# Optimization experiments

Hardware: AMD Instinct MI355X
Metric: run time of the kernel (lower is better)

Reference implementation:

```python
import jax, jax.numpy as jnp
import numpy as np

N, E, D, H, C = 50000, 250000, 300, 4, 75  # nodes, edges, in_size=300, heads=4, out=75 (H*C=300)


def setup_inputs() -> dict:
    key = jax.random.key(0)
    ks = jax.random.split(key, 32)
    rn = lambda k, shape, s=0.05: jax.random.normal(k, shape, jnp.float32) * s
    inp = {}
    inp['x'] = rn(ks[0], (N, D), 1.0)
    inp['edge_index'] = jax.random.randint(ks[1], (2, E), 0, N, dtype=jnp.int32)
    inp['edge_attr'] = rn(ks[2], (E, 4), 1.0)
    inp['obj_normals'] = rn(ks[3], (N, 3), 1.0)
    # parameters (Linear stored as [in, out] so y = x @ W + b)
    inp['Wq'] = rn(ks[4], (D, H * C)); inp['bq'] = rn(ks[5], (H * C,))
    inp['Wk'] = rn(ks[6], (D, H * C)); inp['bk'] = rn(ks[7], (H * C,))
    inp['Wv'] = rn(ks[8], (D, H * C)); inp['bv'] = rn(ks[9], (H * C,))
    inp['We'] = rn(ks[10], (D, H * C))               # lin_edge, no bias
    inp['Wn'] = rn(ks[11], (3, D)); inp['bn'] = rn(ks[12], (D,))      # map_normal
    inp['Wxy'] = rn(ks[13], (2, D)); inp['bxy'] = rn(ks[14], (D,))    # map_xy_relative_coord
    inp['Wloc'] = rn(ks[15], (3 * D, D)); inp['bloc'] = rn(ks[16], (D,))  # map_back_edge_loc
    inp['Wobj'] = rn(ks[17], (2 * D, D)); inp['bobj'] = rn(ks[18], (D,))  # map_back_edge_obj
    inp['Wfus'] = rn(ks[19], (2 * D, D)); inp['bfus'] = rn(ks[20], (D,))  # hv_words_fusion
    inp['Wcls'] = rn(ks[21], (D, 5)); inp['bcls'] = rn(ks[22], (5,))      # horizontal_word_cls
    inp['Wskip'] = rn(ks[23], (D, H * C)); inp['bskip'] = rn(ks[24], (H * C,))  # lin_skip
    inp['vocab'] = rn(ks[25], (7, D), 1.0)  # spatial_vocab_we
    return inp


def reference(x, edge_index, edge_attr, obj_normals,
              Wq, bq, Wk, bk, Wv, bv, We, Wn, bn, Wxy, bxy,
              Wloc, bloc, Wobj, bobj, Wfus, bfus, Wcls, bcls,
              Wskip, bskip, vocab):
    src, dst = edge_index[0], edge_index[1]  # x_j = x[src], x_i = x[dst]
    x_i = x[dst]
    x_j = x[src]
    q = (x_i @ Wq + bq).reshape(E, H, C)
    k = (x_j @ Wk + bk).reshape(E, H, C)
    # vertical (top/bottom) word embeddings gated by edge_attr signs
    top = (edge_attr[:, 0] > 0).astype(x.dtype)[:, None] * vocab[0][None, :]
    bot = (edge_attr[:, 1] < 0).astype(x.dtype)[:, None] * vocab[1][None, :]
    vert = top + bot                                           # [E, D]
    # horizontal word probabilities from geometry + feature cues
    ni = obj_normals[dst] @ Wn + bn
    nj = obj_normals[src] @ Wn + bn
    xy = edge_attr[:, 2:4] @ Wxy + bxy
    loc = jnp.concatenate([xy, ni, nj], axis=1) @ Wloc + bloc
    obj = jnp.concatenate([x_i, x_j - x_i], axis=1) @ Wobj + bobj
    prob = jax.nn.softmax(jnp.tanh(obj + loc) @ Wcls + bcls, axis=1)   # [E, 5]
    horiz = prob @ vocab[2:7]                                  # [E, D]
    edge_word = jnp.concatenate([vert, horiz], axis=1) @ Wfus + bfus   # [E, D]
    ef = (edge_word @ We).reshape(E, H, C)                     # lin_edge
    k = k + ef
    # scaled dot-product attention with per-destination-node softmax
    alpha = (q * k).sum(-1) / jnp.asarray(np.sqrt(C), x.dtype)  # [E, H]
    m = jax.ops.segment_max(alpha, dst, num_segments=N)
    alpha = jnp.exp(alpha - m[dst])
    den = jax.ops.segment_sum(alpha, dst, num_segments=N)
    alpha = alpha / den[dst]
    v = (x_j @ Wv + bv).reshape(E, H, C) + ef
    msg = v * alpha[..., None]                                  # [E, H, C]
    out = jax.ops.segment_sum(msg, dst, num_segments=N).reshape(N, H * C)
    out = out + x @ Wskip + bskip                               # concat heads + root skip
    return out
```

## Files before the change

### kernel.cpp

```cpp
#include <hip/hip_runtime.h>
#include <hip/hip_bf16.h>
#include <math.h>

#define NDIM 300
#define KPAD 320
#define NREAL 1800
#define NPAD 1920

typedef __hip_bfloat16 bf16;
typedef __attribute__((ext_vector_type(8))) short short8;
typedef __attribute__((ext_vector_type(4))) float f32x4;

__device__ __forceinline__ void gl_lds16(const void* g, void* l) {
    __builtin_amdgcn_global_load_lds(
        (const __attribute__((address_space(1))) void*)g,
        (__attribute__((address_space(3))) void*)l, 16, 0, 0);
}

__device__ __forceinline__ float bflo(uint u) { return __uint_as_float(u << 16); }
__device__ __forceinline__ float bfhi(uint u) { return __uint_as_float(u & 0xFFFF0000u); }

__global__ void small_pre(
    const float* __restrict__ Wn, const float* __restrict__ bn,
    const float* __restrict__ Wxy, const float* __restrict__ bxy,
    const float* __restrict__ Wloc, const float* __restrict__ bloc,
    const float* __restrict__ bobj,
    const float* __restrict__ Wfus,
    const float* __restrict__ vocab,
    float* __restrict__ Wn1, float* __restrict__ Wn2,
    float* __restrict__ Mxy, float* __restrict__ bgeo,
    float* __restrict__ vf5, float* __restrict__ t0, float* __restrict__ t1)
{
    int i = blockIdx.x * blockDim.x + threadIdx.x;
    if (i < 900) {
        int r = i / 300, c = i % 300;
        float s = 0.f;
        for (int k = 0; k < 300; k++) s += Wn[r*300+k] * Wloc[(300+k)*300+c];
        Wn1[i] = s;
    } else if (i < 1800) {
        int j = i - 900; int r = j/300, c = j%300;
        float s = 0.f;
        for (int k = 0; k < 300; k++) s += Wn[r*300+k] * Wloc[(600+k)*300+c];
        Wn2[j] = s;
    } else if (i < 2400) {
        int j = i - 1800; int r = j/300, c = j%300;
        float s = 0.f;
        for (int k = 0; k < 300; k++) s += Wxy[r*300+k] * Wloc[k*300+c];
        Mxy[j] = 2.f * s;
    } else if (i < 2700) {
        int c = i - 2400;
        float s = bloc[c] + bobj[c];
        for (int k = 0; k < 300; k++) s += bxy[k] * Wloc[k*300+c];
        for (int k = 0; k < 300; k++) s += bn[k] * (Wloc[(300+k)*300+c] + Wloc[(600+k)*300+c]);
        bgeo[c] = 2.f * s;
    } else if (i < 4200) {
        int j = i - 2700; int p = j/300, c = j%300;
        float s = 0.f;
        for (int k = 0; k < 300; k++) s += vocab[(2+p)*300+k] * Wfus[(300+k)*300+c];
        vf5[j] = s;
    } else if (i < 4500) {
        int c = i - 4200;
        float s = 0.f;
        for (int k = 0; k < 300; k++) s += vocab[k] * Wfus[k*300+c];
        t0[c] = s;
    } else if (i < 4800) {
        int c = i - 4500;
        float s = 0.f;
        for (int k = 0; k < 300; k++) s += vocab[300+k] * Wfus[k*300+c];
        t1[c] = s;
    }
}

__global__ void small_pre2(
    const float* __restrict__ We, const float* __restrict__ bfus,
    const float* __restrict__ vf5, const float* __restrict__ t0, const float* __restrict__ t1,
    const float* __restrict__ Wcls,
    float* __restrict__ E8, float* __restrict__ WclsT)
{
    int i = blockIdx.x * blockDim.x + threadIdx.x;
    if (i < 2400) {
        int r = i / 300, c = i % 300;
        const float* src;
        if (r == 0) src = t0;
        else if (r == 1) src = t1;
        else if (r == 7) src = bfus;
        else src = vf5 + (r - 2) * 300;
        float s = 0.f;
        for (int k = 0; k < 300; k++) s += src[k] * We[k*300+c];
        E8[i] = s;
    } else if (i < 3900) {
        int j = i - 2400; int cl = j / 300, c = j % 300;
        WclsT[cl * 300 + c] = Wcls[c * 5 + cl];
    }
}

__global__ void pack_w(
    const float* __restrict__ Wq, const float* __restrict__ Wk,
    const float* __restrict__ Wv, const float* __restrict__ Wskip,
    const float* __restrict__ Wobj,
    const float* __restrict__ Wn1, const float* __restrict__ Wn2,
    const float* __restrict__ bq, const float* __restrict__ bk,
    const float* __restrict__ bv, const float* __restrict__ bskip,
    bf16* __restrict__ WcatT, float* __restrict__ bcat)
{
    int i = blockIdx.x * blockDim.x + threadIdx.x;
    if (i < NREAL) {
        int c = i;
        float b = 0.f;
        if (c < 600)       { if (!(c & 1)) b = bq[c >> 1]; }
        else if (c < 1200) { int cc = c - 600; if (cc & 1) b = bk[cc >> 1]; }
        else if (c < 1500) b = bv[c - 1200];
        else               b = bskip[c - 1500];
        bcat[i] = b;
    }
    if (i < NPAD * KPAD) {
        int cp = i / KPAD, k = i % KPAD;
        float v = 0.f;
        if (cp < NREAL) {
            int seg, jj;
            if (cp < 600)       { jj = cp >> 1; seg = (cp & 1) ? 4 : 0; }
            else if (cp < 1200) { int cc = cp - 600; jj = cc >> 1; seg = (cc & 1) ? 1 : 5; }
            else if (cp < 1500) { jj = cp - 1200; seg = 2; }
            else                { jj = cp - 1500; seg = 3; }
            if (k < 300) {
                switch (seg) {
                    case 0: v = Wq[k*300+jj]; break;
                    case 1: v = Wk[k*300+jj]; break;
                    case 2: v = Wv[k*300+jj]; break;
                    case 3: v = Wskip[k*300+jj]; break;
                    case 4: v = Wobj[k*300+jj] - Wobj[(300+k)*300+jj]; break;
                    default: v = Wobj[(300+k)*300+jj]; break;
                }
            } else if (k < 303) {
                if (seg == 4) v = Wn1[(k-300)*300+jj];
                else if (seg == 5) v = Wn2[(k-300)*300+jj];
            }
            if (seg >= 4) v *= 2.f;
        }
        WcatT[i] = __float2bfloat16(v);
    }
}

__global__ void conv_xb(const float* __restrict__ X, const float* __restrict__ Nrm,
                        bf16* __restrict__ Xb, int M)
{
    int i = blockIdx.x * blockDim.x + threadIdx.x;
    int row = i / 40, c8 = i % 40;
    if (row >= M) return;
    int c0 = c8 * 8;
    union { bf16 h[8]; short8 s; } u;
    #pragma unroll
    for (int t = 0; t < 8; t++) {
        int c = c0 + t;
        float v = 0.f;
        if (c < 300)      v = X[(size_t)row * 300 + c];
        else if (c < 303) v = Nrm[(size_t)row * 3 + (c - 300)];
        u.h[t] = __float2bfloat16(v);
    }
    *(short8*)&Xb[(size_t)row * 320 + c0] = u.s;
}

__global__ __launch_bounds__(256) void qe8_k(
    const bf16* __restrict__ QP, const float* __restrict__ E8,
    float* __restrict__ QE8f, int N)
{
    __shared__ unsigned short Qs[64 * 302];
    const int tid = threadIdx.x;
    const int n0 = blockIdx.x * 64;
    const int nrows = min(64, N - n0);
    const int nu = nrows * 300;
    const uint* src = (const uint*)QP + (size_t)n0 * 300;
    for (int i = tid; i < nu; i += 256) {
        int rr = i / 300, cc = i - rr * 300;
        Qs[rr * 302 + cc] = (unsigned short)src[i];
    }
    __syncthreads();
    const int w = tid >> 6, l = tid & 63;
    if (l >= nrows) return;
    float acc[8] = {0.f,0.f,0.f,0.f,0.f,0.f,0.f,0.f};
    const int cb = 75 * w;
    for (int cc = 0; cc < 75; cc++) {
        int c = cb + cc;
        float qv = __uint_as_float(((uint)Qs[l * 302 + c]) << 16);
        #pragma unroll
        for (int s = 0; s < 8; s++) acc[s] += qv * E8[s * 300 + c];
    }
    float* out = QE8f + (size_t)(n0 + l) * 32;
    #pragma unroll
    for (int s = 0; s < 8; s++) out[s * 4 + w] = acc[s];
}

__global__ void hist_k(const int* __restrict__ ei, int* __restrict__ deg, int E) {
    int e = blockIdx.x * blockDim.x + threadIdx.x;
    if (e < E) atomicAdd(&deg[ei[E + e]], 1);
}

__global__ __launch_bounds__(1024) void scan_local(
    const int* __restrict__ deg, int* __restrict__ off, int* __restrict__ bsum, int N)
{
    __shared__ int buf[1024];
    int i = blockIdx.x * 1024 + threadIdx.x;
    int v = (i < N) ? deg[i] : 0;
    buf[threadIdx.x] = v;
    __syncthreads();
    #pragma unroll
    for (int ofs = 1; ofs < 1024; ofs <<= 1) {
        int t = (threadIdx.x >= ofs) ? buf[threadIdx.x - ofs] : 0;
        __syncthreads();
        buf[threadIdx.x] += t;
        __syncthreads();
    }
    if (i < N) off[i] = buf[threadIdx.x] - v;
    if (threadIdx.x == 1023) bsum[blockIdx.x] = buf[1023];
}

__global__ __launch_bounds__(1024) void scan_bsum(
    const int* __restrict__ bsum, int* __restrict__ bexc, int nb)
{
    __shared__ int buf[1024];
    int v = (threadIdx.x < nb) ? bsum[threadIdx.x] : 0;
    buf[threadIdx.x] = v;
    __syncthreads();
    #pragma unroll
    for (int ofs = 1; ofs < 1024; ofs <<= 1) {
        int t = (threadIdx.x >= ofs) ? buf[threadIdx.x - ofs] : 0;
        __syncthreads();
        buf[threadIdx.x] += t;
        __syncthreads();
    }
    if (threadIdx.x < nb) bexc[threadIdx.x] = buf[threadIdx.x] - v;
}

__global__ void scan_add(int* __restrict__ off, int* __restrict__ cur,
                         const int* __restrict__ bexc, int N, int E)
{
    int i = blockIdx.x * blockDim.x + threadIdx.x;
    if (i < N) {
        int o = off[i] + bexc[i >> 10];
        off[i] = o; cur[i] = o;
    }
    if (i == 0) off[N] = E;
}

__global__ void scatter_k(const int* __restrict__ ei, const float* __restrict__ ea,
                          int* __restrict__ cur,
                          int2* __restrict__ esd, float* __restrict__ eas, int E) {
    int e = blockIdx.x * blockDim.x + threadIdx.x;
    if (e < E) {
        int s = ei[e];
        int d = ei[E + e];
        float4 a = *(const float4*)&ea[(size_t)e * 4];
        int p = atomicAdd(&cur[d], 1);
        esd[p] = make_int2(s, d);
        *(float4*)&eas[(size_t)p * 4] = a;
    }
}

__global__ __launch_bounds__(256) void gemm_mfma(
    const bf16* __restrict__ Xb,
    const bf16* __restrict__ Bt, const float* __restrict__ bcat,
    bf16* __restrict__ QP, bf16* __restrict__ PK, bf16* __restrict__ V,
    float* __restrict__ Ot, int M, int npan)
{
    __shared__ __align__(16) char smraw[32768];
    bf16*  Asb = (bf16*)smraw;
    bf16*  Bsb = (bf16*)(smraw + 16384);
    bf16*  EP  = (bf16*)smraw;
    float* EPf = (float*)smraw;

    const int bid = blockIdx.x;
    int p, cx;
    {
        const int full = (npan >> 3) * 120;
        if (bid < full) {
            int g = bid / 120, r = bid - g * 120;
            p = (g << 3) + (r & 7); cx = r >> 3;
        } else {
            int r = bid - full;
            int tp = npan & 7;
            p = (npan & ~7) + r % tp; cx = r / tp;
        }
    }
    const int r0 = p * 128;
    const int c0 = cx * 128;

    const int tid  = threadIdx.x;
    const int wave = tid >> 6;
    const int lane = tid & 63;
    const int wm = (wave >> 1) * 64;
    const int wn = (wave & 1) * 64;
    const int lr = lane & 15;
    const int lq = lane >> 4;

    f32x4 acc[4][4];
    #pragma unroll
    for (int j = 0; j < 4; j++)
        #pragma unroll
        for (int i = 0; i < 4; i++) acc[j][i] = (f32x4){0.f, 0.f, 0.f, 0.f};

    const bf16* aSrc[2];
    const bf16* bSrc[2];
    {
        const int bcol_l = lane >> 2;
        const int bkp    = (lane & 3) * 8;
        #pragma unroll
        for (int h = 0; h < 2; h++) {
            int t = h * 256 + wave * 64 + lane;
            int grow = min(r0 + (t >> 2), M - 1);
            aSrc[h] = Xb + (size_t)grow * 320 + (t & 3) * 8;
            bSrc[h] = Bt + (size_t)(c0 + wave * 32 + h * 16 + bcol_l) * KPAD + bkp;
        }
    }

    auto stage = [&](int buf, int kb) {
        #pragma unroll
        for (int h = 0; h < 2; h++) {
            int tbase = h * 256 + wave * 64;
            gl_lds16(aSrc[h] + kb, &Asb[buf * 4096 + tbase * 8]);
        }
        #pragma unroll
        for (int h = 0; h < 2; h++) {
            int cloc = wave * 32 + h * 16;
            gl_lds16(bSrc[h] + kb, &Bsb[buf * 4096 + cloc * 32]);
        }
    };

    stage(0, 0);
    #pragma unroll
    for (int it = 0; it < 10; it++) {
        __syncthreads();
        if (it < 9) stage((it + 1) & 1, (it + 1) * 32);
        const int b = it & 1;
        short8 af[4], bfr[4];
        #pragma unroll
        for (int i = 0; i < 4; i++)
            af[i] = *(const short8*)&Asb[b * 4096 + (wm + i * 16 + lr) * 32 + lq * 8];
        #pragma unroll
        for (int j = 0; j < 4; j++)
            bfr[j] = *(const short8*)&Bsb[b * 4096 + (wn + j * 16 + lr) * 32 + lq * 8];
        #pragma unroll
        for (int j = 0; j < 4; j++)
            #pragma unroll
            for (int i = 0; i < 4; i++)
                acc[j][i] = __builtin_amdgcn_mfma_f32_16x16x32_bf16(
                    bfr[j], af[i], acc[j][i], 0, 0, 0);
    }

    if (c0 < 1500) {
        #pragma unroll
        for (int hm = 0; hm < 2; hm++) {
            __syncthreads();
            if ((wave >> 1) == hm) {
                #pragma unroll
                for (int j = 0; j < 4; j++) {
                    int colL = wn + j * 16 + lq * 4;
                    float4 bb = *(const float4*)&bcat[c0 + colL];
                    #pragma unroll
                    for (int i = 0; i < 4; i++) {
                        int row = i * 16 + lr;
                        union { bf16 h[4]; uint2 u2; } pk;
                        pk.h[0] = __float2bfloat16(acc[j][i][0] + bb.x);
                        pk.h[1] = __float2bfloat16(acc[j][i][1] + bb.y);
                        pk.h[2] = __float2bfloat16(acc[j][i][2] + bb.z);
                        pk.h[3] = __float2bfloat16(acc[j][i][3] + bb.w);
                        *(uint2*)&EP[row * 136 + colL] = pk.u2;
                    }
                }
            }
            __syncthreads();
            #pragma unroll
            for (int rep = 0; rep < 8; rep++) {
                int row = wave * 16 + rep * 2 + (lane >> 5);
                int gr = r0 + hm * 64 + row;
                int col = c0 + 4 * (lane & 31);
                if (gr < M && col < 1500) {
                    uint2 val = *(const uint2*)&EP[row * 136 + 4 * (lane & 31)];
                    if (col < 600)       *(uint2*)&QP[(size_t)gr * 600 + col] = val;
                    else if (col < 1200) *(uint2*)&PK[(size_t)gr * 600 + (col - 600)] = val;
                    else                 *(uint2*)&V [(size_t)gr * 300 + (col - 1200)] = val;
                }
            }
        }
    }
    if (c0 + 128 > 1500) {
        #pragma unroll
        for (int hm = 0; hm < 2; hm++) {
            #pragma unroll
            for (int h = 0; h < 2; h++) {
                if (c0 + h * 64 + 63 < 1500) continue;
                __syncthreads();
                if ((wave >> 1) == hm && (wave & 1) == h) {
                    #pragma unroll
                    for (int j = 0; j < 4; j++) {
                        int colL = j * 16 + lq * 4;
                        int colb = c0 + h * 64 + colL;
                        if (colb < NREAL) {
                            float4 bb = *(const float4*)&bcat[colb];
                            #pragma unroll
                            for (int i = 0; i < 4; i++) {
                                int row = i * 16 + lr;
                                f32x4 vv;
                                vv[0] = acc[j][i][0] + bb.x;
                                vv[1] = acc[j][i][1] + bb.y;
                                vv[2] = acc[j][i][2] + bb.z;
                                vv[3] = acc[j][i][3] + bb.w;
                                *(f32x4*)&EPf[row * 68 + colL] = vv;
                            }
                        }
                    }
                }
                __syncthreads();
                #pragma unroll
                for (int rep = 0; rep < 16; rep++) {
                    int row = wave * 16 + rep;
                    int gr = r0 + hm * 64 + row;
                    int col = c0 + h * 64 + lane;
                    if (gr < M && col >= 1500 && col < NREAL)
                        Ot[(size_t)gr * 300 + (col - 1500)] = EPf[row * 68 + lane];
                }
            }
        }
    }
}

__global__ __launch_bounds__(256) void edge_alpha(
    const int2* __restrict__ esd, const float* __restrict__ eas,
    const bf16* __restrict__ QP, const bf16* __restrict__ PK,
    const float* __restrict__ Mxy, const float* __restrict__ bgeo,
    const float* __restrict__ QE8f, const float* __restrict__ WclsT,
    const float* __restrict__ bcls,
    float* __restrict__ AW,
    int E, int nwaves)
{
    __shared__ __align__(16) float red[4][20 * 68];
    __shared__ float res[4][20];
    const int wv   = threadIdx.x >> 6;
    const int lane = threadIdx.x & 63;
    float* __restrict__ rw = red[wv];
    float* __restrict__ rs = res[wv];
    const int gw  = blockIdx.x * 4 + wv;
    const int per = (E + nwaves - 1) / nwaves;
    const int t0  = gw * per;
    if (t0 >= E) return;
    const int t1 = min(t0 + per, E);
    const bool ok4 = lane < 44;

    float mx0[5], mx1[5], bg[5], wcl[5][5];
    #pragma unroll
    for (int r = 0; r < 4; r++) {
        int c = lane + 64 * r;
        mx0[r] = Mxy[c]; mx1[r] = Mxy[300 + c]; bg[r] = bgeo[c];
        #pragma unroll
        for (int cl = 0; cl < 5; cl++) wcl[cl][r] = WclsT[cl * 300 + c];
    }
    {
        int c = lane + 256;
        mx0[4] = ok4 ? Mxy[c] : 0.f;
        mx1[4] = ok4 ? Mxy[300 + c] : 0.f;
        bg[4]  = ok4 ? bgeo[c] : 0.f;
        #pragma unroll
        for (int cl = 0; cl < 5; cl++) wcl[cl][4] = ok4 ? WclsT[cl * 300 + c] : 0.f;
    }
    float bc[5];
    #pragma unroll
    for (int cl = 0; cl < 5; cl++) bc[cl] = bcls[cl];
    const float isc = 0.11547005383792516f;

    const uint* QPu = (const uint*)QP;
    const uint* PKu = (const uint*)PK;

    int prev_d = -1;
    float qv[5], pib[5];
    float prt[18];

    auto reload = [&](int dd) {
        const uint* qr = QPu + (size_t)dd * 300 + lane;
        #pragma unroll
        for (int r = 0; r < 4; r++) {
            uint uq = qr[64 * r];
            qv[r] = bflo(uq); pib[r] = bfhi(uq) + bg[r];
        }
        uint uq = ok4 ? qr[256] : 0u;
        qv[4] = bflo(uq); pib[4] = bfhi(uq) + bg[4];
    };
    auto compute = [&](const uint (&pk)[5], float az, float aw_, int ub) {
        float tt[5], qk[5];
        #pragma unroll
        for (int r = 0; r < 5; r++) {
            float pj = bflo(pk[r]), kf = bfhi(pk[r]);
            float v = pib[r] + pj + az * mx0[r] + aw_ * mx1[r];
            tt[r] = fmaf(-2.f, __builtin_amdgcn_rcpf(1.f + __expf(v)), 1.f);
            qk[r] = qv[r] * kf;
        }
        #pragma unroll
        for (int cl = 0; cl < 5; cl++)
            prt[ub + cl] = tt[0]*wcl[cl][0] + tt[1]*wcl[cl][1] + tt[2]*wcl[cl][2]
                         + tt[3]*wcl[cl][3] + tt[4]*wcl[cl][4];
        float h0 = qk[0], h3 = qk[4], h1 = 0.f, h2 = 0.f;
        if (lane < 11) h0 += qk[1]; else h1 += qk[1];
        if (lane < 22) h1 += qk[2]; else h2 += qk[2];
        if (lane < 33) h2 += qk[3]; else h3 += qk[3];
        prt[ub+5] = h0; prt[ub+6] = h1; prt[ub+7] = h2; prt[ub+8] = h3;
    };

    for (int t = t0; t < t1; t += 2) {
        const int i0 = t;
        const int i1 = (t + 1 < t1) ? t + 1 : t;
        const int2 sd0 = esd[i0], sd1 = esd[i1];
        const float4 a40 = *(const float4*)&eas[(size_t)4 * i0];
        const float4 a41 = *(const float4*)&eas[(size_t)4 * i1];

        uint pk0[5], pk1[5];
        const uint* p0r = PKu + (size_t)sd0.x * 300 + lane;
        const uint* p1r = PKu + (size_t)sd1.x * 300 + lane;
        #pragma unroll
        for (int r = 0; r < 4; r++) { pk0[r] = p0r[64 * r]; pk1[r] = p1r[64 * r]; }
        pk0[4] = ok4 ? p0r[256] : 0u;
        pk1[4] = ok4 ? p1r[256] : 0u;

        if (sd0.y != prev_d) reload(sd0.y);
        compute(pk0, a40.z, a40.w, 0);
        if (sd1.y != sd0.y) reload(sd1.y);
        compute(pk1, a41.z, a41.w, 9);
        prev_d = sd1.y;

        #pragma unroll
        for (int v = 0; v < 18; v++) rw[v * 68 + lane] = prt[v];
        #pragma unroll
        for (int i = 0; i < 5; i++) {
            int v = 4 * i + (lane >> 4);
            const f32x4 q4 = *(const f32x4*)&rw[v * 68 + (lane & 15) * 4];
            float s = (q4[0] + q4[1]) + (q4[2] + q4[3]);
            s += __shfl_xor(s, 1, 64);
            s += __shfl_xor(s, 2, 64);
            s += __shfl_xor(s, 4, 64);
            s += __shfl_xor(s, 8, 64);
            if ((lane & 15) == 0 && v < 18) rs[v] = s;
        }
        {
            const int    u  = lane >> 5;
            const int    ub = u * 9;
            const float4 au = u ? a41 : a40;
            const int    dd = u ? sd1.y : sd0.y;
            const int    tw = u ? i1 : i0;
            float lg0 = rs[ub+0] + bc[0], lg1 = rs[ub+1] + bc[1], lg2 = rs[ub+2] + bc[2];
            float lg3 = rs[ub+3] + bc[3], lg4 = rs[ub+4] + bc[4];
            float mxv = fmaxf(fmaxf(fmaxf(lg0, lg1), fmaxf(lg2, lg3)), lg4);
            float p0 = __expf(lg0 - mxv), p1 = __expf(lg1 - mxv), p2 = __expf(lg2 - mxv);
            float p3 = __expf(lg3 - mxv), p4 = __expf(lg4 - mxv);
            float pinv = __builtin_amdgcn_rcpf(p0 + p1 + p2 + p3 + p4);
            p0 *= pinv; p1 *= pinv; p2 *= pinv; p3 *= pinv; p4 *= pinv;
            float ct  = au.x > 0.f ? 1.f : 0.f;
            float cb_ = au.y < 0.f ? 1.f : 0.f;
            const f32x4* qe = (const f32x4*)(QE8f + (size_t)dd * 32);
            f32x4 addv = ct*qe[0] + cb_*qe[1] + p0*qe[2] + p1*qe[3]
                       + p2*qe[4] + p3*qe[5] + p4*qe[6] + qe[7];
            float ax0 = __expf((rs[ub+5] + addv[0]) * isc);
            float ax1 = __expf((rs[ub+6] + addv[1]) * isc);
            float ax2 = __expf((rs[ub+7] + addv[2]) * isc);
            float ax3 = __expf((rs[ub+8] + addv[3]) * isc);
            if ((lane & 31) == 0) {
                float* awp = AW + (size_t)12 * tw;
                *(float4*)(awp)     = make_float4(ax0, ax1, ax2, ax3);
                *(float4*)(awp + 4) = make_float4(ct, cb_, p0, p1);
                *(float4*)(awp + 8) = make_float4(p2, p3, p4, 0.f);
            }
        }
    }
}

__global__ __launch_bounds__(256) void node_pv(
    const int2* __restrict__ esd, const bf16* __restrict__ V,
    const float* __restrict__ E8, const float* __restrict__ AW,
    const int* __restrict__ off,
    float* __restrict__ Ot, int N)
{
    const int wid  = threadIdx.x >> 6;
    const int lane = threadIdx.x & 63;
    const int n = blockIdx.x * 4 + wid;
    if (n >= N) return;
    const int e0 = off[n], e1 = off[n + 1];
    if (e0 == e1) return;
    const size_t nrow = (size_t)n * 300;
    const bool ok4 = lane < 44;

    float e8r[8][5];
    #pragma unroll
    for (int rr = 0; rr < 8; rr++) {
        #pragma unroll
        for (int r = 0; r < 4; r++) e8r[rr][r] = E8[rr * 300 + lane + 64 * r];
        e8r[rr][4] = ok4 ? E8[rr * 300 + lane + 256] : 0.f;
    }

    float macc[5] = {0.f, 0.f, 0.f, 0.f, 0.f};
    float den0 = 0.f, den1 = 0.f, den2 = 0.f, den3 = 0.f;

    auto body = [&](int t) {
        int s = esd[t].x;
        const float* awp = AW + (size_t)12 * t;
        float4 ax = *(const float4*)(awp);
        float4 wa = *(const float4*)(awp + 4);
        float4 wb = *(const float4*)(awp + 8);
        const bf16* vr = V + (size_t)s * 300 + lane;
        #pragma unroll
        for (int r = 0; r < 5; r++) {
            float vv = (r < 4) ? __bfloat162float(vr[64 * r])
                               : (ok4 ? __bfloat162float(vr[256]) : 0.f);
            float efc = wa.x * e8r[0][r] + wa.y * e8r[1][r] + wa.z * e8r[2][r] + wa.w * e8r[3][r]
                      + wb.x * e8r[4][r] + wb.y * e8r[5][r] + wb.z * e8r[6][r] + e8r[7][r];
            float w = (r == 0) ? ax.x
                    : (r == 1) ? (lane < 11 ? ax.x : ax.y)
                    : (r == 2) ? (lane < 22 ? ax.y : ax.z)
                    : (r == 3) ? (lane < 33 ? ax.z : ax.w)
                    : ax.w;
            macc[r] += w * (vv + efc);
        }
        den0 += ax.x; den1 += ax.y; den2 += ax.z; den3 += ax.w;
    };
    int t = e0;
    for (; t + 1 < e1; t += 2) { body(t); body(t + 1); }
    if (t < e1) body(t);

    const float rd0 = __builtin_amdgcn_rcpf(den0);
    const float rd1 = __builtin_amdgcn_rcpf(den1);
    const float rd2 = __builtin_amdgcn_rcpf(den2);
    const float rd3 = __builtin_amdgcn_rcpf(den3);
    #pragma unroll
    for (int r = 0; r < 5; r++) {
        int c = lane + 64 * r;
        if (c < 300) {
            float rd = (r == 0) ? rd0
                     : (r == 1) ? (lane < 11 ? rd0 : rd1)
                     : (r == 2) ? (lane < 22 ? rd1 : rd2)
                     : (r == 3) ? (lane < 33 ? rd2 : rd3)
                     : rd3;
            Ot[nrow + c] += macc[r] * rd;
        }
    }
}

extern "C" void kernel_launch(void* const* d_in, const int* in_sizes, int n_in,
                              void* d_out, int out_size, void* d_ws, size_t ws_size,
                              hipStream_t stream)
{
    const float* x     = (const float*)d_in[0];
    const int*   ei    = (const int*)  d_in[1];
    const float* ea    = (const float*)d_in[2];
    const float* on    = (const float*)d_in[3];
    const float* Wq    = (const float*)d_in[4];
    const float* bq    = (const float*)d_in[5];
    const float* Wk    = (const float*)d_in[6];
    const float* bk    = (const float*)d_in[7];
    const float* Wv    = (const float*)d_in[8];
    const float* bv    = (const float*)d_in[9];
    const float* We    = (const float*)d_in[10];
    const float* Wn    = (const float*)d_in[11];
    const float* bn    = (const float*)d_in[12];
    const float* Wxy   = (const float*)d_in[13];
    const float* bxy   = (const float*)d_in[14];
    const float* Wloc  = (const float*)d_in[15];
    const float* bloc  = (const float*)d_in[16];
    const float* Wobj  = (const float*)d_in[17];
    const float* bobj  = (const float*)d_in[18];
    const float* Wfus  = (const float*)d_in[19];
    const float* bfus  = (const float*)d_in[20];
    const float* Wcls  = (const float*)d_in[21];
    const float* bcls  = (const float*)d_in[22];
    const float* Wskip = (const float*)d_in[23];
    const float* bskip = (const float*)d_in[24];
    const float* vocab = (const float*)d_in[25];

    const int N = in_sizes[0] / NDIM;
    const int E = in_sizes[1] / 2;

    const size_t nodeElems = (size_t)N * 300;
    const size_t wcatElems = (size_t)NPAD * KPAD;
    const size_t xbElems   = (size_t)N * 320;
    size_t xbBytes = xbElems * sizeof(bf16);
    const size_t ovlBytes = ((size_t)16 * E + (size_t)32 * N) * sizeof(float);
    if (ovlBytes > xbBytes) xbBytes = ovlBytes;

    const size_t f32Elems  = NREAL + 904 + 904 + 600 + 304 + 1504 + 304 + 304 + 2400 + 1504;
    const size_t intElems  = (size_t)N + (size_t)(N + 1) + (size_t)N
                           + (size_t)2 * E + 2048;
    size_t need = (5 * nodeElems + wcatElems) * sizeof(bf16) + xbBytes
                + f32Elems * sizeof(float) + intElems * sizeof(int);
    if (ws_size < need) return;

    bf16* wsh = (bf16*)d_ws;
    bf16* QPb   = wsh;
    bf16* PKb   = QPb + (size_t)2 * nodeElems;
    bf16* Vb    = PKb + (size_t)2 * nodeElems;
    bf16* WcatT = Vb + nodeElems;
    bf16* Xb    = WcatT + wcatElems;
    float* AW   = (float*)Xb;
    float* eas  = AW + (size_t)12 * E;
    float* QE8f = eas + (size_t)4 * E;
    float* ws = (float*)((char*)Xb + xbBytes);
    size_t o = 0;
    float* bcat  = ws + o; o += NREAL;
    float* Wn1   = ws + o; o += 904;
    float* Wn2   = ws + o; o += 904;
    float* Mxyb  = ws + o; o += 600;
    float* bgeo  = ws + o; o += 304;
    float* vf5   = ws + o; o += 1504;
    float* t0b   = ws + o; o += 304;
    float* t1b   = ws + o; o += 304;
    float* E8b   = ws + o; o += 2400;
    float* WclsT = ws + o; o += 1504;
    int* ip = (int*)(ws + o);
    int* deg    = ip;             ip += N;
    int* offb   = ip;             ip += N + 1;
    int* curb   = ip;             ip += N;
    int2* esd   = (int2*)ip;      ip += (size_t)2 * E;
    int* bsum   = ip;             ip += 1024;
    int* bexc   = ip;             ip += 1024;
    (void)n_in; (void)out_size;

    hipMemsetAsync(deg, 0, (size_t)N * sizeof(int), stream);

    small_pre<<<19, 256, 0, stream>>>(Wn, bn, Wxy, bxy, Wloc, bloc, bobj, Wfus, vocab,
                                      Wn1, Wn2, Mxyb, bgeo, vf5, t0b, t1b);
    small_pre2<<<16, 256, 0, stream>>>(We, bfus, vf5, t0b, t1b, Wcls, E8b, WclsT);
    pack_w<<<(NPAD * KPAD + 255) / 256, 256, 0, stream>>>(
        Wq, Wk, Wv, Wskip, Wobj, Wn1, Wn2, bq, bk, bv, bskip, WcatT, bcat);
    conv_xb<<<((size_t)N * 40 + 255) / 256, 256, 0, stream>>>(x, on, Xb, N);

    const int ebk = (E + 255) / 256;
    hist_k<<<ebk, 256, 0, stream>>>(ei, deg, E);
    const int nbl = (N + 1023) / 1024;
    scan_local<<<nbl, 1024, 0, stream>>>(deg, offb, bsum, N);
    scan_bsum<<<1, 1024, 0, stream>>>(bsum, bexc, nbl);
    scan_add<<<(N + 255) / 256, 256, 0, stream>>>(offb, curb, bexc, N, E);

    const int npan = (N + 127) / 128;
    gemm_mfma<<<npan * 15, 256, 0, stream>>>(Xb, WcatT, bcat,
                                             QPb, PKb, Vb, (float*)d_out, N, npan);

    scatter_k<<<ebk, 256, 0, stream>>>(ei, ea, curb, esd, eas, E);
    qe8_k<<<(N + 63) / 64, 256, 0, stream>>>(QPb, E8b, QE8f, N);

    const int eab = 2048;
    edge_alpha<<<eab, 256, 0, stream>>>(esd, eas, QPb, PKb,
                                        Mxyb, bgeo, QE8f, WclsT, bcls,
                                        AW, E, eab * 4);

    const int nb = (N + 3) / 4;
    node_pv<<<nb, 256, 0, stream>>>(esd, Vb, E8b, AW,
                                    offb, (float*)d_out, N);
}
```

Baseline: 621.0 us.

## Merge independent preprocessing kernels and unroll node aggregation loop by four

Independent small kernels are merged into combined launches that dispatch on block index: weight precompute with x conversion and the degree histogram, E8/WclsT with weight packing, and the edge scatter with the Q·E8 projection. This cuts launch count and lets unrelated work overlap on the GPU. The node_pv loop is unrolled by four, issuing all V row gathers first to raise memory-level parallelism. The merged scatter/qe8 kernel now reserves shared memory for every block, which may lower occupancy for the scatter part.

```diff
diff --git a/kernel.cpp b/kernel.cpp
--- a/kernel.cpp
+++ b/kernel.cpp
@@ -20,7 +20,7 @@
 __device__ __forceinline__ float bflo(uint u) { return __uint_as_float(u << 16); }
 __device__ __forceinline__ float bfhi(uint u) { return __uint_as_float(u & 0xFFFF0000u); }
 
-__global__ void small_pre(
+__global__ void k1_pre_conv_hist(
     const float* __restrict__ Wn, const float* __restrict__ bn,
     const float* __restrict__ Wxy, const float* __restrict__ bxy,
     const float* __restrict__ Wloc, const float* __restrict__ bloc,
@@ -29,72 +29,77 @@
     const float* __restrict__ vocab,
     float* __restrict__ Wn1, float* __restrict__ Wn2,
     float* __restrict__ Mxy, float* __restrict__ bgeo,
-    float* __restrict__ vf5, float* __restrict__ t0, float* __restrict__ t1)
-{
-    int i = blockIdx.x * blockDim.x + threadIdx.x;
-    if (i < 900) {
-        int r = i / 300, c = i % 300;
-        float s = 0.f;
-        for (int k = 0; k < 300; k++) s += Wn[r*300+k] * Wloc[(300+k)*300+c];
-        Wn1[i] = s;
-    } else if (i < 1800) {
-        int j = i - 900; int r = j/300, c = j%300;
-        float s = 0.f;
-        for (int k = 0; k < 300; k++) s += Wn[r*300+k] * Wloc[(600+k)*300+c];
-        Wn2[j] = s;
-    } else if (i < 2400) {
-        int j = i - 1800; int r = j/300, c = j%300;
-        float s = 0.f;
-        for (int k = 0; k < 300; k++) s += Wxy[r*300+k] * Wloc[k*300+c];
-        Mxy[j] = 2.f * s;
-    } else if (i < 2700) {
-        int c = i - 2400;
-        float s = bloc[c] + bobj[c];
-        for (int k = 0; k < 300; k++) s += bxy[k] * Wloc[k*300+c];
-        for (int k = 0; k < 300; k++) s += bn[k] * (Wloc[(300+k)*300+c] + Wloc[(600+k)*300+c]);
-        bgeo[c] = 2.f * s;
-    } else if (i < 4200) {
-        int j = i - 2700; int p = j/300, c = j%300;
-        float s = 0.f;
-        for (int k = 0; k < 300; k++) s += vocab[(2+p)*300+k] * Wfus[(300+k)*300+c];
-        vf5[j] = s;
-    } else if (i < 4500) {
-        int c = i - 4200;
-        float s = 0.f;
-        for (int k = 0; k < 300; k++) s += vocab[k] * Wfus[k*300+c];
-        t0[c] = s;
-    } else if (i < 4800) {
-        int c = i - 4500;
-        float s = 0.f;
-        for (int k = 0; k < 300; k++) s += vocab[300+k] * Wfus[k*300+c];
-        t1[c] = s;
-    }
-}
-
-__global__ void small_pre2(
+    float* __restrict__ vf5, float* __restrict__ t0, float* __restrict__ t1,
+    const float* __restrict__ X, const float* __restrict__ Nrm,
+    bf16* __restrict__ Xb, int M, int nconv,
+    const int* __restrict__ ei, int* __restrict__ deg, int E)
+{
+    const int bid = blockIdx.x;
+    if (bid < 19) {
+        int i = bid * 256 + threadIdx.x;
+        if (i < 900) {
+            int r = i / 300, c = i % 300;
+            float s = 0.f;
+            for (int k = 0; k < 300; k++) s += Wn[r*300+k] * Wloc[(300+k)*300+c];
+            Wn1[i] = s;
+        } else if (i < 1800) {
+            int j = i - 900; int r = j/300, c = j%300;
+            float s = 0.f;
+            for (int k = 0; k < 300; k++) s += Wn[r*300+k] * Wloc[(600+k)*300+c];
+            Wn2[j] = s;
+        } else if (i < 2400) {
+            int j = i - 1800; int r = j/300, c = j%300;
+            float s = 0.f;
+            for (int k = 0; k < 300; k++) s += Wxy[r*300+k] * Wloc[k*300+c];
+            Mxy[j] = 2.f * s;
+        } else if (i < 2700) {
+            int c = i - 2400;
+            float s = bloc[c] + bobj[c];
+            for (int k = 0; k < 300; k++) s += bxy[k] * Wloc[k*300+c];
+            for (int k = 0; k < 300; k++) s += bn[k] * (Wloc[(300+k)*300+c] + Wloc[(600+k)*300+c]);
+            bgeo[c] = 2.f * s;
+        } else if (i < 4200) {
+            int j = i - 2700; int p = j/300, c = j%300;
+            float s = 0.f;
+            for (int k = 0; k < 300; k++) s += vocab[(2+p)*300+k] * Wfus[(300+k)*300+c];
+            vf5[j] = s;
+        } else if (i < 4500) {
+            int c = i - 4200;
+            float s = 0.f;
+            for (int k = 0; k < 300; k++) s += vocab[k] * Wfus[k*300+c];
+            t0[c] = s;
+        } else if (i < 4800) {
+            int c = i - 4500;
+            float s = 0.f;
+            for (int k = 0; k < 300; k++) s += vocab[300+k] * Wfus[k*300+c];
+            t1[c] = s;
+        }
+    } else if (bid < 19 + nconv) {
+        int i = (bid - 19) * 256 + threadIdx.x;
+        int row = i / 40, c8 = i % 40;
+        if (row >= M) return;
+        int c0 = c8 * 8;
+        union { bf16 h[8]; short8 s; } u;
+        #pragma unroll
+        for (int t = 0; t < 8; t++) {
+            int c = c0 + t;
+            float v = 0.f;
+            if (c < 300)      v = X[(size_t)row * 300 + c];
+            else if (c < 303) v = Nrm[(size_t)row * 3 + (c - 300)];
+            u.h[t] = __float2bfloat16(v);
+        }
+        *(short8*)&Xb[(size_t)row * 320 + c0] = u.s;
+    } else {
+        int e = (bid - 19 - nconv) * 256 + threadIdx.x;
+        if (e < E) atomicAdd(&deg[ei[E + e]], 1);
+    }
+}
+
+__global__ void k2_pre2_pack(
     const float* __restrict__ We, const float* __restrict__ bfus,
     const float* __restrict__ vf5, const float* __restrict__ t0, const float* __restrict__ t1,
     const float* __restrict__ Wcls,
-    float* __restrict__ E8, float* __restrict__ WclsT)
-{
-    int i = blockIdx.x * blockDim.x + threadIdx.x;
-    if (i < 2400) {
-        int r = i / 300, c = i % 300;
-        const float* src;
-        if (r == 0) src = t0;
-        else if (r == 1) src = t1;
-        else if (r == 7) src = bfus;
-        else src = vf5 + (r - 2) * 300;
-        float s = 0.f;
-        for (int k = 0; k < 300; k++) s += src[k] * We[k*300+c];
-        E8[i] = s;
-    } else if (i < 3900) {
-        int j = i - 2400; int cl = j / 300, c = j % 300;
-        WclsT[cl * 300 + c] = Wcls[c * 5 + cl];
-    }
-}
-
-__global__ void pack_w(
+    float* __restrict__ E8, float* __restrict__ WclsT,
     const float* __restrict__ Wq, const float* __restrict__ Wk,
     const float* __restrict__ Wv, const float* __restrict__ Wskip,
     const float* __restrict__ Wobj,
@@ -103,96 +108,61 @@
     const float* __restrict__ bv, const float* __restrict__ bskip,
     bf16* __restrict__ WcatT, float* __restrict__ bcat)
 {
-    int i = blockIdx.x * blockDim.x + threadIdx.x;
-    if (i < NREAL) {
-        int c = i;
-        float b = 0.f;
-        if (c < 600)       { if (!(c & 1)) b = bq[c >> 1]; }
-        else if (c < 1200) { int cc = c - 600; if (cc & 1) b = bk[cc >> 1]; }
-        else if (c < 1500) b = bv[c - 1200];
-        else               b = bskip[c - 1500];
-        bcat[i] = b;
-    }
-    if (i < NPAD * KPAD) {
-        int cp = i / KPAD, k = i % KPAD;
-        float v = 0.f;
-        if (cp < NREAL) {
-            int seg, jj;
-            if (cp < 600)       { jj = cp >> 1; seg = (cp & 1) ? 4 : 0; }
-            else if (cp < 1200) { int cc = cp - 600; jj = cc >> 1; seg = (cc & 1) ? 1 : 5; }
-            else if (cp < 1500) { jj = cp - 1200; seg = 2; }
-            else                { jj = cp - 1500; seg = 3; }
-            if (k < 300) {
-                switch (seg) {
-                    case 0: v = Wq[k*300+jj]; break;
-                    case 1: v = Wk[k*300+jj]; break;
-                    case 2: v = Wv[k*300+jj]; break;
-                    case 3: v = Wskip[k*300+jj]; break;
-                    case 4: v = Wobj[k*300+jj] - Wobj[(300+k)*300+jj]; break;
-                    default: v = Wobj[(300+k)*300+jj]; break;
+    const int bid = blockIdx.x;
+    if (bid < 16) {
+        int i = bid * 256 + threadIdx.x;
+        if (i < 2400) {
+            int r = i / 300, c = i % 300;
+            const float* src;
+            if (r == 0) src = t0;
+            else if (r == 1) src = t1;
+            else if (r == 7) src = bfus;
+            else src = vf5 + (r - 2) * 300;
+            float s = 0.f;
+            for (int k = 0; k < 300; k++) s += src[k] * We[k*300+c];
+            E8[i] = s;
+        } else if (i < 3900) {
+            int j = i - 2400; int cl = j / 300, c = j % 300;
+            WclsT[cl * 300 + c] = Wcls[c * 5 + cl];
+        }
+    } else {
+        int i = (bid - 16) * 256 + threadIdx.x;
+        if (i < NREAL) {
+            int c = i;
+            float b = 0.f;
+            if (c < 600)       { if (!(c & 1)) b = bq[c >> 1]; }
+            else if (c < 1200) { int cc = c - 600; if (cc & 1) b = bk[cc >> 1]; }
+            else if (c < 1500) b = bv[c - 1200];
+            else               b = bskip[c - 1500];
+            bcat[i] = b;
+        }
+        if (i < NPAD * KPAD) {
+            int cp = i / KPAD, k = i % KPAD;
+            float v = 0.f;
+            if (cp < NREAL) {
+                int seg, jj;
+                if (cp < 600)       { jj = cp >> 1; seg = (cp & 1) ? 4 : 0; }
+                else if (cp < 1200) { int cc = cp - 600; jj = cc >> 1; seg = (cc & 1) ? 1 : 5; }
+                else if (cp < 1500) { jj = cp - 1200; seg = 2; }
+                else                { jj = cp - 1500; seg = 3; }
+                if (k < 300) {
+                    switch (seg) {
+                        case 0: v = Wq[k*300+jj]; break;
+                        case 1: v = Wk[k*300+jj]; break;
+                        case 2: v = Wv[k*300+jj]; break;
+                        case 3: v = Wskip[k*300+jj]; break;
+                        case 4: v = Wobj[k*300+jj] - Wobj[(300+k)*300+jj]; break;
+                        default: v = Wobj[(300+k)*300+jj]; break;
+                    }
+                } else if (k < 303) {
+                    if (seg == 4) v = Wn1[(k-300)*300+jj];
+                    else if (seg == 5) v = Wn2[(k-300)*300+jj];
                 }
-            } else if (k < 303) {
-                if (seg == 4) v = Wn1[(k-300)*300+jj];
-                else if (seg == 5) v = Wn2[(k-300)*300+jj];
+                if (seg >= 4) v *= 2.f;
             }
-            if (seg >= 4) v *= 2.f;
-        }
-        WcatT[i] = __float2bfloat16(v);
-    }
-}
-
-__global__ void conv_xb(const float* __restrict__ X, const float* __restrict__ Nrm,
-                        bf16* __restrict__ Xb, int M)
-{
-    int i = blockIdx.x * blockDim.x + threadIdx.x;
-    int row = i / 40, c8 = i % 40;
-    if (row >= M) return;
-    int c0 = c8 * 8;
-    union { bf16 h[8]; short8 s; } u;
-    #pragma unroll
-    for (int t = 0; t < 8; t++) {
-        int c = c0 + t;
-        float v = 0.f;
-        if (c < 300)      v = X[(size_t)row * 300 + c];
-        else if (c < 303) v = Nrm[(size_t)row * 3 + (c - 300)];
-        u.h[t] = __float2bfloat16(v);
-    }
-    *(short8*)&Xb[(size_t)row * 320 + c0] = u.s;
-}
-
-__global__ __launch_bounds__(256) void qe8_k(
-    const bf16* __restrict__ QP, const float* __restrict__ E8,
-    float* __restrict__ QE8f, int N)
-{
-    __shared__ unsigned short Qs[64 * 302];
-    const int tid = threadIdx.x;
-    const int n0 = blockIdx.x * 64;
-    const int nrows = min(64, N - n0);
-    const int nu = nrows * 300;
-    const uint* src = (const uint*)QP + (size_t)n0 * 300;
-    for (int i = tid; i < nu; i += 256) {
-        int rr = i / 300, cc = i - rr * 300;
-        Qs[rr * 302 + cc] = (unsigned short)src[i];
-    }
-    __syncthreads();
-    const int w = tid >> 6, l = tid & 63;
-    if (l >= nrows) return;
-    float acc[8] = {0.f,0.f,0.f,0.f,0.f,0.f,0.f,0.f};
-    const int cb = 75 * w;
-    for (int cc = 0; cc < 75; cc++) {
-        int c = cb + cc;
-        float qv = __uint_as_float(((uint)Qs[l * 302 + c]) << 16);
-        #pragma unroll
-        for (int s = 0; s < 8; s++) acc[s] += qv * E8[s * 300 + c];
-    }
-    float* out = QE8f + (size_t)(n0 + l) * 32;
-    #pragma unroll
-    for (int s = 0; s < 8; s++) out[s * 4 + w] = acc[s];
-}
-
-__global__ void hist_k(const int* __restrict__ ei, int* __restrict__ deg, int E) {
-    int e = blockIdx.x * blockDim.x + threadIdx.x;
-    if (e < E) atomicAdd(&deg[ei[E + e]], 1);
+            WcatT[i] = __float2bfloat16(v);
+        }
+    }
 }
 
 __global__ __launch_bounds__(1024) void scan_local(
@@ -240,20 +210,6 @@
         off[i] = o; cur[i] = o;
     }
     if (i == 0) off[N] = E;
-}
-
-__global__ void scatter_k(const int* __restrict__ ei, const float* __restrict__ ea,
-                          int* __restrict__ cur,
-                          int2* __restrict__ esd, float* __restrict__ eas, int E) {
-    int e = blockIdx.x * blockDim.x + threadIdx.x;
-    if (e < E) {
-        int s = ei[e];
-        int d = ei[E + e];
-        float4 a = *(const float4*)&ea[(size_t)e * 4];
-        int p = atomicAdd(&cur[d], 1);
-        esd[p] = make_int2(s, d);
-        *(float4*)&eas[(size_t)p * 4] = a;
-    }
 }
 
 __global__ __launch_bounds__(256) void gemm_mfma(
@@ -423,6 +379,52 @@
     }
 }
 
+__global__ __launch_bounds__(256) void k3_scatter_qe8(
+    const int* __restrict__ ei, const float* __restrict__ ea,
+    int* __restrict__ cur,
+    int2* __restrict__ esd, float* __restrict__ eas, int E, int ebk,
+    const bf16* __restrict__ QP, const float* __restrict__ E8,
+    float* __restrict__ QE8f, int N)
+{
+    __shared__ unsigned short Qs[64 * 302];
+    const int bid = blockIdx.x;
+    if (bid < ebk) {
+        int e = bid * 256 + threadIdx.x;
+        if (e < E) {
+            int s = ei[e];
+            int d = ei[E + e];
+            float4 a = *(const float4*)&ea[(size_t)e * 4];
+            int p = atomicAdd(&cur[d], 1);
+            esd[p] = make_int2(s, d);
+            *(float4*)&eas[(size_t)p * 4] = a;
+        }
+        return;
+    }
+    const int tid = threadIdx.x;
+    const int n0 = (bid - ebk) * 64;
+    const int nrows = min(64, N - n0);
+    const int nu = nrows * 300;
+    const uint* src = (const uint*)QP + (size_t)n0 * 300;
+    for (int i = tid; i < nu; i += 256) {
+        int rr = i / 300, cc = i - rr * 300;
+        Qs[rr * 302 + cc] = (unsigned short)src[i];
+    }
+    __syncthreads();
+    const int w = tid >> 6, l = tid & 63;
+    if (l >= nrows) return;
+    float acc[8] = {0.f,0.f,0.f,0.f,0.f,0.f,0.f,0.f};
+    const int cb = 75 * w;
+    for (int cc = 0; cc < 75; cc++) {
+        int c = cb + cc;
+        float qv = __uint_as_float(((uint)Qs[l * 302 + c]) << 16);
+        #pragma unroll
+        for (int s = 0; s < 8; s++) acc[s] += qv * E8[s * 300 + c];
+    }
+    float* out = QE8f + (size_t)(n0 + l) * 32;
+    #pragma unroll
+    for (int s = 0; s < 8; s++) out[s * 4 + w] = acc[s];
+}
+
 __global__ __launch_bounds__(256) void edge_alpha(
     const int2* __restrict__ esd, const float* __restrict__ eas,
     const bf16* __restrict__ QP, const bf16* __restrict__ PK,
@@ -595,7 +597,41 @@
     float macc[5] = {0.f, 0.f, 0.f, 0.f, 0.f};
     float den0 = 0.f, den1 = 0.f, den2 = 0.f, den3 = 0.f;
 
-    auto body = [&](int t) {
+    int t = e0;
+    for (; t + 4 <= e1; t += 4) {
+        int s4[4];
+        #pragma unroll
+        for (int u = 0; u < 4; u++) s4[u] = esd[t + u].x;
+        float vv[4][5];
+        #pragma unroll
+        for (int u = 0; u < 4; u++) {
+            const bf16* vr = V + (size_t)s4[u] * 300 + lane;
+            #pragma unroll
+            for (int r = 0; r < 4; r++) vv[u][r] = __bfloat162float(vr[64 * r]);
+            vv[u][4] = ok4 ? __bfloat162float(vr[256]) : 0.f;
+        }
+        #pragma unroll
+        for (int u = 0; u < 4; u++) {
+            const float* awp = AW + (size_t)12 * (t + u);
+            float4 ax = *(const float4*)(awp);
+            float4 wa = *(const float4*)(awp + 4);
+            float4 wb = *(const float4*)(awp + 8);
+            #pragma unroll
+            for (int r = 0; r < 5; r++) {
+                float efc = wa.x * e8r[0][r] + wa.y * e8r[1][r] + wa.z * e8r[2][r]
+                          + wa.w * e8r[3][r] + wb.x * e8r[4][r] + wb.y * e8r[5][r]
+                          + wb.z * e8r[6][r] + e8r[7][r];
+                float w = (r == 0) ? ax.x
+                        : (r == 1) ? (lane < 11 ? ax.x : ax.y)
+                        : (r == 2) ? (lane < 22 ? ax.y : ax.z)
+                        : (r == 3) ? (lane < 33 ? ax.z : ax.w)
+                        : ax.w;
+                macc[r] += w * (vv[u][r] + efc);
+            }
+            den0 += ax.x; den1 += ax.y; den2 += ax.z; den3 += ax.w;
+        }
+    }
+    for (; t < e1; t++) {
         int s = esd[t].x;
         const float* awp = AW + (size_t)12 * t;
         float4 ax = *(const float4*)(awp);
@@ -604,22 +640,20 @@
         const bf16* vr = V + (size_t)s * 300 + lane;
         #pragma unroll
         for (int r = 0; r < 5; r++) {
-            float vv = (r < 4) ? __bfloat162float(vr[64 * r])
-                               : (ok4 ? __bfloat162float(vr[256]) : 0.f);
-            float efc = wa.x * e8r[0][r] + wa.y * e8r[1][r] + wa.z * e8r[2][r] + wa.w * e8r[3][r]
-                      + wb.x * e8r[4][r] + wb.y * e8r[5][r] + wb.z * e8r[6][r] + e8r[7][r];
+            float vvs = (r < 4) ? __bfloat162float(vr[64 * r])
+                                : (ok4 ? __bfloat162float(vr[256]) : 0.f);
+            float efc = wa.x * e8r[0][r] + wa.y * e8r[1][r] + wa.z * e8r[2][r]
+                      + wa.w * e8r[3][r] + wb.x * e8r[4][r] + wb.y * e8r[5][r]
+                      + wb.z * e8r[6][r] + e8r[7][r];
             float w = (r == 0) ? ax.x
                     : (r == 1) ? (lane < 11 ? ax.x : ax.y)
                     : (r == 2) ? (lane < 22 ? ax.y : ax.z)
                     : (r == 3) ? (lane < 33 ? ax.z : ax.w)
                     : ax.w;
-            macc[r] += w * (vv + efc);
+            macc[r] += w * (vvs + efc);
         }
         den0 += ax.x; den1 += ax.y; den2 += ax.z; den3 += ax.w;
-    };
-    int t = e0;
-    for (; t + 1 < e1; t += 2) { body(t); body(t + 1); }
-    if (t < e1) body(t);
+    }
 
     const float rd0 = __builtin_amdgcn_rcpf(den0);
     const float rd1 = __builtin_amdgcn_rcpf(den1);
@@ -719,15 +753,17 @@
 
     hipMemsetAsync(deg, 0, (size_t)N * sizeof(int), stream);
 
-    small_pre<<<19, 256, 0, stream>>>(Wn, bn, Wxy, bxy, Wloc, bloc, bobj, Wfus, vocab,
-                                      Wn1, Wn2, Mxyb, bgeo, vf5, t0b, t1b);
-    small_pre2<<<16, 256, 0, stream>>>(We, bfus, vf5, t0b, t1b, Wcls, E8b, WclsT);
-    pack_w<<<(NPAD * KPAD + 255) / 256, 256, 0, stream>>>(
+    const int ebk   = (E + 255) / 256;
+    const int nconv = ((int)((size_t)N * 40) + 255) / 256;
+
+    k1_pre_conv_hist<<<19 + nconv + ebk, 256, 0, stream>>>(
+        Wn, bn, Wxy, bxy, Wloc, bloc, bobj, Wfus, vocab,
+        Wn1, Wn2, Mxyb, bgeo, vf5, t0b, t1b,
+        x, on, Xb, N, nconv, ei, deg, E);
+    k2_pre2_pack<<<16 + (NPAD * KPAD + 255) / 256, 256, 0, stream>>>(
+        We, bfus, vf5, t0b, t1b, Wcls, E8b, WclsT,
         Wq, Wk, Wv, Wskip, Wobj, Wn1, Wn2, bq, bk, bv, bskip, WcatT, bcat);
-    conv_xb<<<((size_t)N * 40 + 255) / 256, 256, 0, stream>>>(x, on, Xb, N);
-
-    const int ebk = (E + 255) / 256;
-    hist_k<<<ebk, 256, 0, stream>>>(ei, deg, E);
+
     const int nbl = (N + 1023) / 1024;
     scan_local<<<nbl, 1024, 0, stream>>>(deg, offb, bsum, N);
     scan_bsum<<<1, 1024, 0, stream>>>(bsum, bexc, nbl);
@@ -737,8 +773,8 @@
     gemm_mfma<<<npan * 15, 256, 0, stream>>>(Xb, WcatT, bcat,
                                              QPb, PKb, Vb, (float*)d_out, N, npan);
 
-    scatter_k<<<ebk, 256, 0, stream>>>(ei, ea, curb, esd, eas, E);
-    qe8_k<<<(N + 63) / 64, 256, 0, stream>>>(QPb, E8b, QE8f, N);
+    k3_scatter_qe8<<<ebk + (N + 63) / 64, 256, 0, stream>>>(
+        ei, ea, curb, esd, eas, E, ebk, QPb, E8b, QE8f, N);
 
     const int eab = 2048;
     edge_alpha<<<eab, 256, 0, stream>>>(esd, eas, QPb, PKb,
```

After: 618.7 us. Within noise of the previous version (-0.4%).
